# Kernel tuning notes

Hardware: AMD Instinct MI355X
Metric: run time of the kernel (lower is better)

The kernel has to match this reference:

```python
import jax, jax.numpy as jnp
import numpy as np

B, NODES, D, DEG = 256, 124, 32, 16
N = B * NODES
EP = NODES * DEG
E = B * EP
L, H, C = 3, 4, 32
NCLS = 40
TMP = 124 + 32 * 2 * L
EPS = 1e-5
NEG_SLOPE = 0.2


def setup_inputs() -> dict:
    key = jax.random.key(0)
    ks = jax.random.split(key, 16)
    x = jax.random.normal(ks[0], (N, D), dtype=jnp.float32)
    # per-graph random edges, guaranteed no self-loops
    src = jax.random.randint(ks[1], (B, EP), 0, NODES)
    off = jax.random.randint(ks[2], (B, EP), 1, NODES)
    dst = (src + off) % NODES
    goff = (jnp.arange(B) * NODES)[:, None]
    edge_index = jnp.stack([(src + goff).reshape(-1), (dst + goff).reshape(-1)]).astype(jnp.int32)
    batch = jnp.repeat(jnp.arange(B), NODES).astype(jnp.int32)
    conv_W = jax.random.normal(ks[3], (L, D, H * C), dtype=jnp.float32) / np.sqrt(D)
    conv_att_l = jax.random.normal(ks[4], (L, H, C), dtype=jnp.float32) * 0.1
    conv_att_r = jax.random.normal(ks[5], (L, H, C), dtype=jnp.float32) * 0.1
    conv_bias = jnp.zeros((L, C), dtype=jnp.float32)
    bn_gamma = jnp.ones((L, C), dtype=jnp.float32)
    bn_beta = jnp.zeros((L, C), dtype=jnp.float32)
    lin1_W = jax.random.normal(ks[6], (NODES * C, 124), dtype=jnp.float32) / np.sqrt(NODES * C)
    lin1_b = jnp.zeros((124,), dtype=jnp.float32)
    bn1_gamma = jnp.ones((124,), dtype=jnp.float32)
    bn1_beta = jnp.zeros((124,), dtype=jnp.float32)
    lin2_W = jax.random.normal(ks[7], (TMP, NCLS), dtype=jnp.float32) / np.sqrt(TMP)
    lin2_b = jnp.zeros((NCLS,), dtype=jnp.float32)
    return dict(x=x, edge_index=edge_index, batch=batch, conv_W=conv_W,
                conv_att_l=conv_att_l, conv_att_r=conv_att_r, conv_bias=conv_bias,
                bn_gamma=bn_gamma, bn_beta=bn_beta, lin1_W=lin1_W, lin1_b=lin1_b,
                bn1_gamma=bn1_gamma, bn1_beta=bn1_beta, lin2_W=lin2_W, lin2_b=lin2_b)


def _supergat_mx(x, src, dst, W, att_l, att_r, bias):
    # SuperGATConv, attention_type='MX', concat=False (mean over heads), eval mode
    h = (x @ W).reshape(N, H, C)              # [N,H,C]
    x_j = h[src]                              # source / message features [E',H,C]
    x_i = h[dst]                              # target features
    logits = jnp.sum(x_i * x_j, -1)           # [E',H] dot-product logits
    alpha = jnp.sum(x_j * att_l, -1) + jnp.sum(x_i * att_r, -1)
    alpha = alpha * jax.nn.sigmoid(logits)
    alpha = jax.nn.leaky_relu(alpha, NEG_SLOPE)
    # scatter-softmax over incoming edges of each target node
    amax = jax.ops.segment_max(alpha, dst, num_segments=N)
    ex = jnp.exp(alpha - amax[dst])
    denom = jax.ops.segment_sum(ex, dst, num_segments=N)
    a = ex / (denom[dst] + 1e-16)             # [E',H]
    out = jax.ops.segment_sum(x_j * a[..., None], dst, num_segments=N)  # [N,H,C]
    return out.mean(axis=1) + bias            # concat=False -> head mean, [N,C]


def _batchnorm(x, gamma, beta):
    mu = x.mean(0)
    var = x.var(0)
    return (x - mu) * jax.lax.rsqrt(var + EPS) * gamma + beta


def reference(x, edge_index, batch, conv_W, conv_att_l, conv_att_r, conv_bias,
              bn_gamma, bn_beta, lin1_W, lin1_b, bn1_gamma, bn1_beta, lin2_W, lin2_b):
    # add self loops once (input edges contain none)
    sl = jnp.arange(N, dtype=edge_index.dtype)
    src = jnp.concatenate([edge_index[0], sl])
    dst = jnp.concatenate([edge_index[1], sl])
    inter = []
    for l in range(L):
        x = _supergat_mx(x, src, dst, conv_W[l], conv_att_l[l], conv_att_r[l], conv_bias[l])
        x = _batchnorm(x, bn_gamma[l], bn_beta[l])
        x = jax.nn.relu(x)
        cnt = jax.ops.segment_sum(jnp.ones((N,), x.dtype), batch, num_segments=B)
        gmean = jax.ops.segment_sum(x, batch, num_segments=B) / cnt[:, None]
        gmax = jax.ops.segment_max(x, batch, num_segments=B)
        inter.append(jnp.concatenate([gmean, gmax], 1))   # [B, 2C]
    x = x.reshape(B, NODES * C)
    x = x @ lin1_W + lin1_b
    x = _batchnorm(x, bn1_gamma, bn1_beta)
    x = jnp.concatenate([x] + inter, 1)                   # inter_connect=True
    x = jax.nn.relu(x)
    return x @ lin2_W + lin2_b                            # [B, NCLS]
```

## Files before the change

kernel.cpp:

```cpp
#include <hip/hip_runtime.h>
#include <math.h>

#define NN 31744
#define NE 507904
#define EP 1984
#define NODES 124
#define NB 256
#define CC 32
#define HC 128
#define FEAT_DIM 316
#define NCLS 40
#define NC 3968
#define EXCAP 192

typedef __attribute__((ext_vector_type(8))) short bf16x8;
typedef __attribute__((ext_vector_type(4))) float f32x4;

#define LOG2E  1.44269504f
#define LOG2E5 0.28853901f

__device__ __forceinline__ unsigned short f2bf(float f) {
    unsigned u = __float_as_uint(f);
    u = u + 0x7FFFu + ((u >> 16) & 1u);
    return (unsigned short)(u >> 16);
}
__device__ __forceinline__ float bf2f(unsigned short s) {
    return __uint_as_float(((unsigned)s) << 16);
}

__global__ __launch_bounds__(256) void mask_build(const int* __restrict__ ei,
                                                  unsigned* __restrict__ gmask,
                                                  int* __restrict__ gdst,
                                                  int* __restrict__ gdent,
                                                  float* __restrict__ bnacc) {
    __shared__ unsigned mcnt[NODES * NODES];
    __shared__ int cnt[128], pref[128];
    __shared__ int locs[124][8];
    int g = blockIdx.x, t = threadIdx.x;
    if (g == 0 && t < 192) bnacc[t] = 0.f;
    for (int i = t; i < NODES * NODES; i += 256) mcnt[i] = 0u;
    __syncthreads();
    for (int e = t; e < EP; e += 256) {
        int s = ei[g * EP + e] - g * NODES;
        int d = ei[NE + g * EP + e] - g * NODES;
        atomicAdd(&mcnt[d * NODES + s], 1u);
    }
    __syncthreads();
    int nd = 0;
    if (t < 124) {
        unsigned m[4] = {0u, 0u, 0u, 0u};
        for (int s = 0; s < NODES; ++s) {
            unsigned c = mcnt[t * NODES + s] + (s == t ? 1u : 0u);
            if (c) {
                m[s >> 5] |= 1u << (s & 31);
                if (c > 1u && nd < 8) { locs[t][nd] = (s << 8) | (int)c; nd++; }
            }
        }
        uint4 mm; mm.x = m[0]; mm.y = m[1]; mm.z = m[2]; mm.w = m[3];
        *(uint4*)&gmask[(size_t)(g * NODES + t) * 4] = mm;
        cnt[t] = nd;
    } else if (t < 128) cnt[t] = 0;
    __syncthreads();
    if (t < 128) pref[t] = cnt[t];
    __syncthreads();
    for (int off = 1; off < 128; off <<= 1) {
        int v = (t >= off && t < 128) ? pref[t - off] : 0;
        __syncthreads();
        if (t < 128) pref[t] += v;
        __syncthreads();
    }
    if (t < 124) {
        int off = pref[t] - cnt[t];
        gdst[g * 132 + t] = off < EXCAP ? off : EXCAP;
        for (int j = 0; j < nd; ++j)
            if (off + j < EXCAP) gdent[g * EXCAP + off + j] = locs[t][j];
    }
    if (t == 0) {
        int tot = pref[127];
        gdst[g * 132 + 124] = tot < EXCAP ? tot : EXCAP;
    }
}

#define HS 136
#define TS 136
#define XS 40
#define ABS 136
#define PWS 40

__global__ __launch_bounds__(1024, 1) void conv_graph(
    const float* __restrict__ xin, const float* __restrict__ W,
    const float* __restrict__ attl, const float* __restrict__ attr,
    const float* __restrict__ bias,
    const unsigned* __restrict__ gmask, const int* __restrict__ gdst,
    const int* __restrict__ gdent,
    float* __restrict__ y, float* __restrict__ bnacc) {

    __shared__ short hbh[128 * HS];
    __shared__ short hbl[128 * HS];
    __shared__ short hTall[128 * TS];
    __shared__ short pwbuf[16 * 1280];
    __shared__ short attBuf[16 * ABS];
    __shared__ float ALs[4][128], ARs[4][128];
    __shared__ unsigned mask[128][4];
    __shared__ unsigned short dupst[136];
    __shared__ unsigned dupent[EXCAP];
    __shared__ float bias_s[32];
    __shared__ float bsum[8][32], bsq[8][32];

    int g = blockIdx.x, t = threadIdx.x, base = g * NODES;
    short* xh  = pwbuf;
    short* xl  = pwbuf + 5120;
    short* WTh = hTall;
    short* WTl = hTall + 5120;

    {
        const float4* xsrc = (const float4*)(xin + (size_t)base * CC);
        for (int i = t; i < 992; i += 1024) {
            float4 v = xsrc[i];
            int n = i >> 3, c4 = i & 7;
            unsigned short h0 = f2bf(v.x), h1 = f2bf(v.y), h2 = f2bf(v.z), h3 = f2bf(v.w);
            unsigned short l0 = f2bf(v.x - bf2f(h0)), l1 = f2bf(v.y - bf2f(h1));
            unsigned short l2 = f2bf(v.z - bf2f(h2)), l3 = f2bf(v.w - bf2f(h3));
            uint2 ph; ph.x = ((unsigned)h1 << 16) | h0; ph.y = ((unsigned)h3 << 16) | h2;
            uint2 pl; pl.x = ((unsigned)l1 << 16) | l0; pl.y = ((unsigned)l3 << 16) | l2;
            *(uint2*)&xh[n * XS + c4 * 4] = ph;
            *(uint2*)&xl[n * XS + c4 * 4] = pl;
        }
        if (t < 4 * XS) { xh[124 * XS + t] = 0; xl[124 * XS + t] = 0; }
    }
    {
        int hc = t & 127, mq = t >> 7, ks = mq * 4;
        unsigned short hh4[4], ll4[4];
#pragma unroll
        for (int q = 0; q < 4; ++q) {
            float w = W[(ks + q) * HC + hc];
            hh4[q] = f2bf(w);
            ll4[q] = f2bf(w - bf2f(hh4[q]));
        }
        uint2 ph; ph.x = ((unsigned)hh4[1] << 16) | hh4[0]; ph.y = ((unsigned)hh4[3] << 16) | hh4[2];
        uint2 pl; pl.x = ((unsigned)ll4[1] << 16) | ll4[0]; pl.y = ((unsigned)ll4[3] << 16) | ll4[2];
        *(uint2*)&WTh[hc * XS + ks] = ph;
        *(uint2*)&WTl[hc * XS + ks] = pl;
    }
    for (int i = t; i < 2048; i += 1024) {
        int n = i >> 7, k = i & 127;
        float v = 0.f;
        int hidx = n & 3;
        if (n < 8 && (k >> 5) == hidx)
            v = (n < 4) ? attl[hidx * 32 + (k & 31)] : attr[hidx * 32 + (k & 31)];
        attBuf[n * ABS + k] = (short)f2bf(v);
    }
    if (t < CC) bias_s[t] = bias[t];
    if (t < 128) {
        if (t < 124) {
            uint4 m = *(const uint4*)&gmask[(size_t)(base + t) * 4];
            mask[t][0] = m.x; mask[t][1] = m.y; mask[t][2] = m.z; mask[t][3] = m.w;
        } else { mask[t][0] = 0u; mask[t][1] = 0u; mask[t][2] = 0u; mask[t][3] = 0u; }
    }
    if (t < 136) dupst[t] = (unsigned short)gdst[g * 132 + (t < 124 ? t : 124)];
    if (t >= 832 && t < 832 + EXCAP) dupent[t - 832] = (unsigned)gdent[g * EXCAP + (t - 832)];
    __syncthreads();

    int wv = t >> 6, l = t & 63;
    int l15 = l & 15, l4 = l >> 4;

#pragma unroll
    for (int j = 0; j < 4; ++j) {
        int idx = wv * 4 + j;
        int tr = idx >> 3, tc = idx & 7;
        bf16x8 ah = *(bf16x8*)&xh[(tr * 16 + l15) * XS + l4 * 8];
        bf16x8 al_ = *(bf16x8*)&xl[(tr * 16 + l15) * XS + l4 * 8];
        bf16x8 bh = *(bf16x8*)&WTh[(tc * 16 + l15) * XS + l4 * 8];
        bf16x8 bl_ = *(bf16x8*)&WTl[(tc * 16 + l15) * XS + l4 * 8];
        f32x4 z = {0.f, 0.f, 0.f, 0.f};
        f32x4 c0 = __builtin_amdgcn_mfma_f32_16x16x32_bf16(ah, bh, z, 0, 0, 0);
        f32x4 c1 = __builtin_amdgcn_mfma_f32_16x16x32_bf16(ah, bl_, z, 0, 0, 0);
        f32x4 c2 = __builtin_amdgcn_mfma_f32_16x16x32_bf16(al_, bh, z, 0, 0, 0);
        f32x4 c = (c0 + c1) + c2;
        int hc = tc * 16 + l15;
#pragma unroll
        for (int r = 0; r < 4; ++r) {
            int n = tr * 16 + l4 * 4 + r;
            float s = c[r];
            unsigned short hi = f2bf(s);
            hbh[n * HS + hc] = (short)hi;
            hbl[n * HS + hc] = (short)f2bf(s - bf2f(hi));
        }
    }
    __syncthreads();

    if (wv < 8) {
        f32x4 c = {0.f, 0.f, 0.f, 0.f};
#pragma unroll
        for (int kb = 0; kb < 4; ++kb) {
            bf16x8 a = *(bf16x8*)&hbh[(wv * 16 + l15) * HS + kb * 32 + l4 * 8];
            bf16x8 b = *(bf16x8*)&attBuf[l15 * ABS + kb * 32 + l4 * 8];
            c = __builtin_amdgcn_mfma_f32_16x16x32_bf16(a, b, c, 0, 0, 0);
        }
        if (l15 < 8) {
#pragma unroll
            for (int r = 0; r < 4; ++r) {
                int n = wv * 16 + l4 * 4 + r;
                if (l15 < 4) ALs[l15][n] = c[r];
                else         ARs[l15 - 4][n] = c[r];
            }
        }
    }
#pragma unroll
    for (int hh2 = 0; hh2 < 4; ++hh2) {
        int k = t & 31, n4 = t >> 5;
        unsigned short r4[4];
#pragma unroll
        for (int r = 0; r < 4; ++r)
            r4[r] = (unsigned short)hbh[(n4 * 4 + r) * HS + hh2 * 32 + k];
        uint2 pk;
        pk.x = ((unsigned)r4[1] << 16) | r4[0];
        pk.y = ((unsigned)r4[3] << 16) | r4[2];
        *(uint2*)&hTall[(hh2 * 32 + k) * TS + n4 * 4] = pk;
    }
    __syncthreads();

    int DJ = wv >> 1;
    float accA[4] = {0.f, 0.f, 0.f, 0.f};
    float accB[4] = {0.f, 0.f, 0.f, 0.f};
    {
        int hh0 = (wv & 1) * 2;
        short* pwb = pwbuf + wv * 1280;
        int dst = DJ * 16 + l15;
        uint4 mrow = *(uint4*)&mask[dst][0];
        unsigned mwords[4] = {mrow.x, mrow.y, mrow.z, mrow.w};
        unsigned cntp[8];
#pragma unroll
        for (int SI = 0; SI < 8; ++SI) {
            unsigned mw = (mwords[SI >> 1] >> ((SI & 1) * 16 + l4 * 4)) & 0xFu;
            cntp[SI] = (mw & 1u) | ((mw & 2u) << 7) | ((mw & 4u) << 14) | ((mw & 8u) << 21);
        }
        {
            int s0 = dupst[dst], s1 = dupst[dst + 1];
            for (int e = s0; e < s1; ++e) {
                unsigned ent = dupent[e];
                unsigned src = (ent >> 8) & 255u;
                unsigned SI = src >> 4;
                unsigned r = (src & 15u) - (unsigned)(l4 * 4);
                if (r < 4u) {
                    unsigned sh = 8u * r;
                    cntp[SI] = (cntp[SI] & ~(255u << sh)) | ((ent & 255u) << sh);
                }
            }
        }

#define GRAM(kb, slot) { \
    _Pragma("unroll") \
    for (int s2 = 0; s2 < 2; ++s2) { \
        int SI = (kb) * 2 + s2; \
        int ao = (SI * 16 + l15) * HS + hh * 32 + l4 * 8; \
        bf16x8 ah = *(bf16x8*)&hbh[ao]; \
        bf16x8 al_ = *(bf16x8*)&hbl[ao]; \
        f32x4 z2 = {0.f, 0.f, 0.f, 0.f}; \
        f32x4 c0 = __builtin_amdgcn_mfma_f32_16x16x32_bf16(ah, gb, z2, 0, 0, 0); \
        f32x4 c1 = __builtin_amdgcn_mfma_f32_16x16x32_bf16(ah, gl, z2, 0, 0, 0); \
        f32x4 c2 = __builtin_amdgcn_mfma_f32_16x16x32_bf16(al_, gb, z2, 0, 0, 0); \
        f32x4 c = (c0 + c1) + c2; \
        int src0 = SI * 16 + l4 * 4; \
        float4 al4 = *(float4*)&ALs[hh][src0]; \
        unsigned cp = cntp[SI]; \
        float pv[4]; \
        _Pragma("unroll") \
        for (int r = 0; r < 4; ++r) { \
            float e2 = __builtin_amdgcn_exp2f(-LOG2E * c[r]); \
            float sig = __builtin_amdgcn_rcpf(1.f + e2); \
            float a2 = (((const float*)&al4)[r] + ar) * sig; \
            float m = fmaxf(a2 * LOG2E, a2 * LOG2E5); \
            float cr = (float)((cp >> (8 * r)) & 255u); \
            pv[r] = __builtin_amdgcn_exp2f(m) * cr; \
        } \
        sden += (pv[0] + pv[1]) + (pv[2] + pv[3]); \
        unsigned w0_, w1_; \
        asm("v_cvt_pk_bf16_f32 %0, %1, %2" : "=v"(w0_) : "v"(pv[0]), "v"(pv[1])); \
        asm("v_cvt_pk_bf16_f32 %0, %1, %2" : "=v"(w1_) : "v"(pv[2]), "v"(pv[3])); \
        uint2 pk_; pk_.x = w0_; pk_.y = w1_; \
        *(uint2*)&pwb[(slot) * 640 + l15 * PWS + s2 * 16 + l4 * 4] = pk_; \
    } }

#define PVOP(kb, slot) { \
    bf16x8 a = *(bf16x8*)&pwb[(slot) * 640 + l15 * PWS + l4 * 8]; \
    bf16x8 b0 = *(bf16x8*)&hTall[(hh * 32 + l15) * TS + (kb) * 32 + l4 * 8]; \
    bf16x8 b1 = *(bf16x8*)&hTall[(hh * 32 + 16 + l15) * TS + (kb) * 32 + l4 * 8]; \
    num0 = __builtin_amdgcn_mfma_f32_16x16x32_bf16(a, b0, num0, 0, 0, 0); \
    num1 = __builtin_amdgcn_mfma_f32_16x16x32_bf16(a, b1, num1, 0, 0, 0); }

#pragma unroll
        for (int jj = 0; jj < 2; ++jj) {
            int hh = hh0 + jj;
            bf16x8 gb = *(bf16x8*)&hbh[dst * HS + hh * 32 + l4 * 8];
            bf16x8 gl = *(bf16x8*)&hbl[dst * HS + hh * 32 + l4 * 8];
            float ar = ARs[hh][dst];
            float sden = 0.f;
            f32x4 num0 = {0.f, 0.f, 0.f, 0.f};
            f32x4 num1 = {0.f, 0.f, 0.f, 0.f};
            GRAM(0, 0);
            GRAM(1, 1); PVOP(0, 0);
            GRAM(2, 0); PVOP(1, 1);
            GRAM(3, 1); PVOP(2, 0);
            PVOP(3, 1);
            sden += __shfl_xor(sden, 16, 64);
            sden += __shfl_xor(sden, 32, 64);
#pragma unroll
            for (int r = 0; r < 4; ++r) {
                float dn = __shfl(sden, l4 * 4 + r, 64) + 1e-16f;
                accA[r] += ((float*)&num0)[r] / dn;
                accB[r] += ((float*)&num1)[r] / dn;
            }
        }
#undef GRAM
#undef PVOP
    }
    __syncthreads();

    float* exch = (float*)pwbuf;
    if (wv & 1) {
#pragma unroll
        for (int r = 0; r < 4; ++r) {
            exch[DJ * 512 + l15 * 16 + l4 * 4 + r] = accA[r];
            exch[DJ * 512 + 256 + l15 * 16 + l4 * 4 + r] = accB[r];
        }
    }
    __syncthreads();

    if (!(wv & 1)) {
        float sA = 0.f, qA = 0.f, sB = 0.f, qB = 0.f;
#pragma unroll
        for (int r = 0; r < 4; ++r) {
            int n = DJ * 16 + l4 * 4 + r;
            float a = accA[r] + exch[DJ * 512 + l15 * 16 + l4 * 4 + r];
            float b = accB[r] + exch[DJ * 512 + 256 + l15 * 16 + l4 * 4 + r];
            a = 0.25f * a + bias_s[l15];
            b = 0.25f * b + bias_s[16 + l15];
            if (n < NODES) {
                y[(size_t)(base + n) * CC + l15] = a;
                y[(size_t)(base + n) * CC + 16 + l15] = b;
                sA += a; qA += a * a; sB += b; qB += b * b;
            }
        }
        sA += __shfl_xor(sA, 16, 64); sA += __shfl_xor(sA, 32, 64);
        qA += __shfl_xor(qA, 16, 64); qA += __shfl_xor(qA, 32, 64);
        sB += __shfl_xor(sB, 16, 64); sB += __shfl_xor(sB, 32, 64);
        qB += __shfl_xor(qB, 16, 64); qB += __shfl_xor(qB, 32, 64);
        if (l < 16) {
            bsum[DJ][l15] = sA; bsum[DJ][16 + l15] = sB;
            bsq[DJ][l15] = qA;  bsq[DJ][16 + l15] = qB;
        }
    }
    __syncthreads();
    if (t < CC) {
        float S = 0.f, Q = 0.f;
#pragma unroll
        for (int w = 0; w < 8; ++w) { S += bsum[w][t]; Q += bsq[w][t]; }
        atomicAdd(&bnacc[t], S);
        atomicAdd(&bnacc[CC + t], Q);
    }
}

__global__ void bn_relu_pool(const float* __restrict__ y, const float* __restrict__ acc,
                             const float* __restrict__ gamma, const float* __restrict__ beta,
                             float* __restrict__ xout, float* __restrict__ feat, int l) {
    int g = blockIdx.x;
    int t = threadIdx.x;
    int c = t & 31, r0 = t >> 5;
    float mu = acc[c] * (1.f / NN);
    float var = acc[32 + c] * (1.f / NN) - mu * mu;
    float sc = rsqrtf(var + 1e-5f) * gamma[c];
    float bt = beta[c];
    float s = 0.f, mx = -INFINITY;
    for (int r = r0; r < NODES; r += 4) {
        int i = (g * NODES + r) * CC + c;
        float v = (y[i] - mu) * sc + bt;
        v = fmaxf(v, 0.f);
        xout[i] = v;
        s += v; mx = fmaxf(mx, v);
    }
    __shared__ float ls[128], lm[128];
    ls[t] = s; lm[t] = mx;
    __syncthreads();
    if (t < 32) {
        float S = ls[t] + ls[32 + t] + ls[64 + t] + ls[96 + t];
        float M = fmaxf(fmaxf(lm[t], lm[32 + t]), fmaxf(lm[64 + t], lm[96 + t]));
        float* fp = feat + g * FEAT_DIM + NODES + l * 64;
        fp[t] = S * (1.f / NODES);
        fp[32 + t] = M;
    }
}

#define L1_GPB 4
#define L1_KS 16
#define L1_KCH 248
__global__ void lin1_part(const float* __restrict__ X, const float* __restrict__ W,
                          float* __restrict__ part) {
    int ks = blockIdx.x & (L1_KS - 1);
    int gb = (blockIdx.x >> 4) * L1_GPB;
    int t = threadIdx.x;
    int kbeg = ks * L1_KCH;
    __shared__ float xs[L1_GPB][124];
    float acc[L1_GPB] = {0.f, 0.f, 0.f, 0.f};
    for (int k0 = kbeg; k0 < kbeg + L1_KCH; k0 += 124) {
        __syncthreads();
        if (t < 124) {
#pragma unroll
            for (int rr = 0; rr < L1_GPB; ++rr) xs[rr][t] = X[(gb + rr) * NC + k0 + t];
        }
        __syncthreads();
        if (t < 124) {
#pragma unroll 4
            for (int kk = 0; kk < 124; ++kk) {
                float w = W[(k0 + kk) * 124 + t];
#pragma unroll
                for (int rr = 0; rr < L1_GPB; ++rr) acc[rr] += xs[rr][kk] * w;
            }
        }
    }
    if (t < 124)
#pragma unroll
        for (int rr = 0; rr < L1_GPB; ++rr)
            part[(ks * NB + gb + rr) * 124 + t] = acc[rr];
}

__global__ void lin1_reduce(const float* __restrict__ part, const float* __restrict__ b,
                            float* __restrict__ out1) {
    int i = blockIdx.x * blockDim.x + threadIdx.x;
    if (i >= NB * 124) return;
    int j = i % 124;
    float s = b[j];
#pragma unroll
    for (int ks = 0; ks < L1_KS; ++ks) s += part[ks * NB * 124 + i];
    out1[i] = s;
}

__global__ void bn1_relu(const float* __restrict__ out1, const float* __restrict__ gamma,
                         const float* __restrict__ beta, float* __restrict__ feat) {
    __shared__ float ps[4][124], pq[4][124], smu[124], ssc[124], sbt[124];
    int t = threadIdx.x;
    int c = t & 127, seg = t >> 7;
    float s = 0.f, q = 0.f;
    if (c < 124) {
        for (int b = seg * 64; b < seg * 64 + 64; ++b) {
            float v = out1[b * 124 + c]; s += v; q += v * v;
        }
        ps[seg][c] = s; pq[seg][c] = q;
    }
    __syncthreads();
    if (t < 124) {
        float S = ps[0][t] + ps[1][t] + ps[2][t] + ps[3][t];
        float Q = pq[0][t] + pq[1][t] + pq[2][t] + pq[3][t];
        float mu = S * (1.f / NB);
        float var = Q * (1.f / NB) - mu * mu;
        smu[t] = mu; ssc[t] = rsqrtf(var + 1e-5f) * gamma[t]; sbt[t] = beta[t];
    }
    __syncthreads();
    if (c < 124) {
        for (int b = seg * 64; b < seg * 64 + 64; ++b) {
            float v = (out1[b * 124 + c] - smu[c]) * ssc[c] + sbt[c];
            feat[b * FEAT_DIM + c] = fmaxf(v, 0.f);
        }
    }
}

__global__ void lin2_k(const float* __restrict__ feat, const float* __restrict__ W,
                       const float* __restrict__ b, float* __restrict__ out) {
    __shared__ float psum[8][40];
    int g = blockIdx.x;
    int t = threadIdx.x;
    int j = t % 40, u = t / 40;
    if (u < 8) {
        int k0 = u * 40, k1 = (u == 7) ? FEAT_DIM : k0 + 40;
        float s = 0.f;
        for (int k = k0; k < k1; ++k) s += feat[g * FEAT_DIM + k] * W[k * NCLS + j];
        psum[u][j] = s;
    }
    __syncthreads();
    if (t < NCLS) {
        float s = b[t];
#pragma unroll
        for (int u2 = 0; u2 < 8; ++u2) s += psum[u2][t];
        out[g * NCLS + t] = s;
    }
}

extern "C" void kernel_launch(void* const* d_in, const int* in_sizes, int n_in,
                              void* d_out, int out_size, void* d_ws, size_t ws_size,
                              hipStream_t stream) {
    const float* x      = (const float*)d_in[0];
    const int*   ei     = (const int*)d_in[1];
    const float* conv_W = (const float*)d_in[3];
    const float* att_l  = (const float*)d_in[4];
    const float* att_r  = (const float*)d_in[5];
    const float* conv_b = (const float*)d_in[6];
    const float* bn_g   = (const float*)d_in[7];
    const float* bn_b   = (const float*)d_in[8];
    const float* lin1_W = (const float*)d_in[9];
    const float* lin1_b = (const float*)d_in[10];
    const float* bn1_g  = (const float*)d_in[11];
    const float* bn1_b  = (const float*)d_in[12];
    const float* lin2_W = (const float*)d_in[13];
    const float* lin2_b = (const float*)d_in[14];

    float* ws = (float*)d_ws;
    float* y     = ws;
    float* xbuf  = y + (size_t)NN * CC;
    float* bnacc = xbuf + (size_t)NN * CC;
    float* feat  = bnacc + 192;
    float* out1  = feat + NB * FEAT_DIM;
    float* part  = out1 + NB * 124;
    unsigned* gmask = (unsigned*)(part + L1_KS * NB * 124);
    int* gdst  = (int*)(gmask + (size_t)NN * 4);
    int* gdent = gdst + NB * 132;

    mask_build<<<NB, 256, 0, stream>>>(ei, gmask, gdst, gdent, bnacc);

    const float* xin = x;
    for (int l = 0; l < 3; ++l) {
        conv_graph<<<NB, 1024, 0, stream>>>(xin, conv_W + l * CC * HC,
                                            att_l + l * HC, att_r + l * HC,
                                            conv_b + l * CC, gmask, gdst, gdent,
                                            y, bnacc + l * 64);
        bn_relu_pool<<<NB, 128, 0, stream>>>(y, bnacc + l * 64, bn_g + l * CC,
                                             bn_b + l * CC, xbuf, feat, l);
        xin = xbuf;
    }

    lin1_part<<<(NB / L1_GPB) * L1_KS, 128, 0, stream>>>(xbuf, lin1_W, part);
    lin1_reduce<<<(NB * 124 + 255) / 256, 256, 0, stream>>>(part, lin1_b, out1);
    bn1_relu<<<1, 512, 0, stream>>>(out1, bn1_g, bn1_b, feat);
    lin2_k<<<NB, 320, 0, stream>>>(feat, lin2_W, lin2_b, (float*)d_out);
}
```

Measured before the change: 154.9 us.

## Fuse BN/ReLU/pooling into next conv prologue and run lin1 on bf16 MFMA

For layers 1 and 2, the batchnorm, ReLU and graph mean/max pooling of the previous layer now run inside the next conv_graph kernel as it loads its node features. Pooling uses shared-memory atomics. This drops two bn_relu_pool launches and the extra write and read of an intermediate activation buffer. The final layer's activations are written as bf16, and lin1 becomes an MFMA kernel with a 4-way K split. A new transpose kernel converts lin1_W to bf16 on every call. The lin1 inputs and weights lose precision compared with the fp32 FMA version, and the shared atomics add some contention.

Result: faster. 145.6 us (median of 2 runs) (-6.0%).

```diff
diff --git a/kernel.cpp b/kernel.cpp
--- a/kernel.cpp
+++ b/kernel.cpp
@@ -81,6 +81,23 @@
     }
 }
 
+__global__ __launch_bounds__(256) void wtrans(const float* __restrict__ W,
+                                              unsigned short* __restrict__ WT) {
+    __shared__ float tile[32][33];
+    int kb = blockIdx.x, jb = blockIdx.y;
+    int t = threadIdx.x;
+    int tr = t >> 5, tc = t & 31;
+    for (int r = tr; r < 32; r += 8) {
+        int k = kb * 32 + r, j = jb * 32 + tc;
+        tile[r][tc] = (j < 124) ? W[k * 124 + j] : 0.f;
+    }
+    __syncthreads();
+    for (int r = tr; r < 32; r += 8) {
+        int j = jb * 32 + r, k = kb * 32 + tc;
+        WT[(size_t)j * NC + k] = f2bf(tile[tc][r]);
+    }
+}
+
 #define HS 136
 #define TS 136
 #define XS 40
@@ -93,6 +110,8 @@
     const float* __restrict__ bias,
     const unsigned* __restrict__ gmask, const int* __restrict__ gdst,
     const int* __restrict__ gdent,
+    const float* __restrict__ bnprev, const float* __restrict__ gprev,
+    const float* __restrict__ bprev, float* __restrict__ feat, int lprev,
     float* __restrict__ y, float* __restrict__ bnacc) {
 
     __shared__ short hbh[128 * HS];
@@ -106,6 +125,8 @@
     __shared__ unsigned dupent[EXCAP];
     __shared__ float bias_s[32];
     __shared__ float bsum[8][32], bsq[8][32];
+    __shared__ float pmean[32];
+    __shared__ int pmax[32];
 
     int g = blockIdx.x, t = threadIdx.x, base = g * NODES;
     short* xh  = pwbuf;
@@ -113,11 +134,30 @@
     short* WTh = hTall;
     short* WTl = hTall + 5120;
 
+    if (t < 32) { pmean[t] = 0.f; pmax[t] = 0; }
+    __syncthreads();
+
     {
         const float4* xsrc = (const float4*)(xin + (size_t)base * CC);
         for (int i = t; i < 992; i += 1024) {
             float4 v = xsrc[i];
             int n = i >> 3, c4 = i & 7;
+            if (lprev >= 0) {
+                float vv[4] = {v.x, v.y, v.z, v.w};
+#pragma unroll
+                for (int q = 0; q < 4; ++q) {
+                    int c = c4 * 4 + q;
+                    float mu = bnprev[c] * (1.f / NN);
+                    float var = bnprev[32 + c] * (1.f / NN) - mu * mu;
+                    float sc = rsqrtf(var + 1e-5f) * gprev[c];
+                    float xv = (vv[q] - mu) * sc + bprev[c];
+                    xv = fmaxf(xv, 0.f);
+                    vv[q] = xv;
+                    atomicAdd(&pmean[c], xv);
+                    atomicMax(&pmax[c], __float_as_int(xv));
+                }
+                v.x = vv[0]; v.y = vv[1]; v.z = vv[2]; v.w = vv[3];
+            }
             unsigned short h0 = f2bf(v.x), h1 = f2bf(v.y), h2 = f2bf(v.z), h3 = f2bf(v.w);
             unsigned short l0 = f2bf(v.x - bf2f(h0)), l1 = f2bf(v.y - bf2f(h1));
             unsigned short l2 = f2bf(v.z - bf2f(h2)), l3 = f2bf(v.w - bf2f(h3));
@@ -160,6 +200,12 @@
     if (t < 136) dupst[t] = (unsigned short)gdst[g * 132 + (t < 124 ? t : 124)];
     if (t >= 832 && t < 832 + EXCAP) dupent[t - 832] = (unsigned)gdent[g * EXCAP + (t - 832)];
     __syncthreads();
+
+    if (lprev >= 0 && t < 32) {
+        float* fp = feat + g * FEAT_DIM + NODES + lprev * 64;
+        fp[t] = pmean[t] * (1.f / NODES);
+        fp[32 + t] = __int_as_float(pmax[t]);
+    }
 
     int wv = t >> 6, l = t & 63;
     int l15 = l & 15, l4 = l >> 4;
@@ -363,7 +409,7 @@
 
 __global__ void bn_relu_pool(const float* __restrict__ y, const float* __restrict__ acc,
                              const float* __restrict__ gamma, const float* __restrict__ beta,
-                             float* __restrict__ xout, float* __restrict__ feat, int l) {
+                             unsigned short* __restrict__ xbf, float* __restrict__ feat, int l) {
     int g = blockIdx.x;
     int t = threadIdx.x;
     int c = t & 31, r0 = t >> 5;
@@ -376,7 +422,7 @@
         int i = (g * NODES + r) * CC + c;
         float v = (y[i] - mu) * sc + bt;
         v = fmaxf(v, 0.f);
-        xout[i] = v;
+        xbf[i] = f2bf(v);
         s += v; mx = fmaxf(mx, v);
     }
     __shared__ float ls[128], lm[128];
@@ -391,37 +437,35 @@
     }
 }
 
-#define L1_GPB 4
-#define L1_KS 16
-#define L1_KCH 248
-__global__ void lin1_part(const float* __restrict__ X, const float* __restrict__ W,
-                          float* __restrict__ part) {
-    int ks = blockIdx.x & (L1_KS - 1);
-    int gb = (blockIdx.x >> 4) * L1_GPB;
+#define L1_KS 4
+#define L1_KC 992
+#define XP 1000
+__global__ __launch_bounds__(512) void lin1_mfma(const unsigned short* __restrict__ Xb,
+                                                 const unsigned short* __restrict__ WT,
+                                                 float* __restrict__ part) {
+    __shared__ unsigned short Xs[16 * XP];
+    int mt = blockIdx.x >> 2, kp = blockIdx.x & 3;
     int t = threadIdx.x;
-    int kbeg = ks * L1_KCH;
-    __shared__ float xs[L1_GPB][124];
-    float acc[L1_GPB] = {0.f, 0.f, 0.f, 0.f};
-    for (int k0 = kbeg; k0 < kbeg + L1_KCH; k0 += 124) {
-        __syncthreads();
-        if (t < 124) {
-#pragma unroll
-            for (int rr = 0; rr < L1_GPB; ++rr) xs[rr][t] = X[(gb + rr) * NC + k0 + t];
-        }
-        __syncthreads();
-        if (t < 124) {
+    int wv = t >> 6, l = t & 63, l15 = l & 15, l4 = l >> 4;
+    int M0 = mt * 16, k0 = kp * L1_KC;
+    for (int i = t; i < 16 * 124; i += 512) {
+        int r = i / 124, c = i - r * 124;
+        *(uint4*)&Xs[r * XP + c * 8] = *(const uint4*)&Xb[(size_t)(M0 + r) * NC + k0 + c * 8];
+    }
+    __syncthreads();
+    int N0 = wv * 16;
+    f32x4 acc = {0.f, 0.f, 0.f, 0.f};
 #pragma unroll 4
-            for (int kk = 0; kk < 124; ++kk) {
-                float w = W[(k0 + kk) * 124 + t];
-#pragma unroll
-                for (int rr = 0; rr < L1_GPB; ++rr) acc[rr] += xs[rr][kk] * w;
-            }
-        }
-    }
-    if (t < 124)
-#pragma unroll
-        for (int rr = 0; rr < L1_GPB; ++rr)
-            part[(ks * NB + gb + rr) * 124 + t] = acc[rr];
+    for (int kk = 0; kk < 31; ++kk) {
+        bf16x8 a = *(bf16x8*)&Xs[l15 * XP + kk * 32 + l4 * 8];
+        bf16x8 b = *(const bf16x8*)&WT[(size_t)(N0 + l15) * NC + k0 + kk * 32 + l4 * 8];
+        acc = __builtin_amdgcn_mfma_f32_16x16x32_bf16(a, b, acc, 0, 0, 0);
+    }
+    if (N0 + l15 < 124) {
+#pragma unroll
+        for (int r = 0; r < 4; ++r)
+            part[(size_t)kp * NB * 124 + (M0 + l4 * 4 + r) * 124 + N0 + l15] = acc[r];
+    }
 }
 
 __global__ void lin1_reduce(const float* __restrict__ part, const float* __restrict__ b,
@@ -504,30 +548,36 @@
     const float* lin2_b = (const float*)d_in[14];
 
     float* ws = (float*)d_ws;
-    float* y     = ws;
-    float* xbuf  = y + (size_t)NN * CC;
-    float* bnacc = xbuf + (size_t)NN * CC;
+    float* y = ws;
+    unsigned short* xbf = (unsigned short*)(y + (size_t)NN * CC);
+    float* bnacc = (float*)(xbf + (size_t)NN * CC);
     float* feat  = bnacc + 192;
     float* out1  = feat + NB * FEAT_DIM;
     float* part  = out1 + NB * 124;
-    unsigned* gmask = (unsigned*)(part + L1_KS * NB * 124);
+    unsigned short* WT = (unsigned short*)(part + L1_KS * NB * 124);
+    unsigned* gmask = (unsigned*)(WT + (size_t)128 * NC);
     int* gdst  = (int*)(gmask + (size_t)NN * 4);
     int* gdent = gdst + NB * 132;
 
     mask_build<<<NB, 256, 0, stream>>>(ei, gmask, gdst, gdent, bnacc);
+    wtrans<<<dim3(NC / 32, 4), 256, 0, stream>>>(lin1_W, WT);
 
     const float* xin = x;
     for (int l = 0; l < 3; ++l) {
+        const float* bnprev = (l == 0) ? nullptr : bnacc + (l - 1) * 64;
+        const float* gprev  = (l == 0) ? bn_g : bn_g + (l - 1) * CC;
+        const float* bprev  = (l == 0) ? bn_b : bn_b + (l - 1) * CC;
         conv_graph<<<NB, 1024, 0, stream>>>(xin, conv_W + l * CC * HC,
                                             att_l + l * HC, att_r + l * HC,
                                             conv_b + l * CC, gmask, gdst, gdent,
+                                            bnprev, gprev, bprev, feat, l - 1,
                                             y, bnacc + l * 64);
-        bn_relu_pool<<<NB, 128, 0, stream>>>(y, bnacc + l * 64, bn_g + l * CC,
-                                             bn_b + l * CC, xbuf, feat, l);
-        xin = xbuf;
-    }
-
-    lin1_part<<<(NB / L1_GPB) * L1_KS, 128, 0, stream>>>(xbuf, lin1_W, part);
+        xin = y;
+    }
+
+    bn_relu_pool<<<NB, 128, 0, stream>>>(y, bnacc + 128, bn_g + 2 * CC, bn_b + 2 * CC,
+                                         xbf, feat, 2);
+    lin1_mfma<<<64, 512, 0, stream>>>(xbf, WT, part);
     lin1_reduce<<<(NB * 124 + 255) / 256, 256, 0, stream>>>(part, lin1_b, out1);
     bn1_relu<<<1, 512, 0, stream>>>(out1, bn1_g, bn1_b, feat);
     lin2_k<<<NB, 320, 0, stream>>>(feat, lin2_W, lin2_b, (float*)d_out);
```
